# Performance work log

Measured on AMD Instinct MI355X. Metric: run time of the kernel, lower is better.

The kernel has to match this reference:

```python
import jax, jax.numpy as jnp
import numpy as np

NUM_HEADS = 16
HEAD_DIM = 64
HIDDEN = 1024


def setup_inputs() -> dict:
    key = jax.random.key(0)
    ks = jax.random.split(key, 5)
    B, L, D = 1, 2048, HIDDEN
    x = jax.random.normal(ks[0], (B, L, D), dtype=jnp.float32)
    # nn.Linear(D, D, bias=False) weights, stored [out, in] like torch
    sc = 1.0 / np.sqrt(D)
    Wq = jax.random.uniform(ks[1], (D, D), jnp.float32, -sc, sc)
    Wk = jax.random.uniform(ks[2], (D, D), jnp.float32, -sc, sc)
    Wv = jax.random.uniform(ks[3], (D, D), jnp.float32, -sc, sc)
    Wo = jax.random.uniform(ks[4], (D, D), jnp.float32, -sc, sc)
    return {"x": x, "Wq": Wq, "Wk": Wk, "Wv": Wv, "Wo": Wo}


def _entmax_naive(scores_raw, mask):
    # scores_raw: [B,H,L,L] unmasked scaled scores (float32); mask: [L,L] bool (True = future/blocked)
    s = jnp.where(mask, -jnp.inf, scores_raw)
    sorted_s = -jnp.sort(-s, axis=-1)                       # descending
    cumsum = jnp.cumsum(sorted_s, axis=-1)
    k = jnp.arange(1, s.shape[-1] + 1, dtype=jnp.float32)
    tau = (cumsum - 1.0) / k
    k_support = jnp.maximum(
        jnp.sum(sorted_s > tau, axis=-1, keepdims=True), 1
    ).astype(jnp.float32)
    # sum over unmasked entries (the -inf masked entries are excluded)
    s_sum = jnp.sum(jnp.where(mask, 0.0, scores_raw), axis=-1, keepdims=True)
    tau_star = (s_sum - 1.0) / k_support
    p = jnp.where(mask, 0.0, jnp.maximum(scores_raw - tau_star, 0.0))
    return p / (jnp.sum(p, axis=-1, keepdims=True) + 1e-10)


def reference(x, Wq, Wk, Wv, Wo):
    B, L, D = x.shape
    H, hd = NUM_HEADS, HEAD_DIM
    q = jnp.einsum('bld,ed->ble', x, Wq).reshape(B, L, H, hd)
    k = jnp.einsum('bld,ed->ble', x, Wk).reshape(B, L, H, hd)
    v = jnp.einsum('bld,ed->ble', x, Wv).reshape(B, L, H, hd)
    scale = hd ** (-0.5)
    scores = jnp.einsum('bihd,bjhd->bhij', q, k).astype(jnp.float32) * scale
    causal_mask = jnp.triu(jnp.ones((L, L), dtype=bool), 1)
    attn = _entmax_naive(scores, causal_mask)               # [B,H,L,L]
    out = jnp.einsum('bhij,bjhd->bihd', attn.astype(x.dtype), v).reshape(B, L, D)
    return jnp.einsum('bld,ed->ble', out, Wo)
```

## Files before the change

### kernel.cpp

```cpp
#include <hip/hip_runtime.h>
#include <hip/hip_bf16.h>

#define CL 2048
#define CD 1024
#define CH 16
#define CHD 64
#define NEGS -1e30f

typedef __attribute__((ext_vector_type(8))) short short8;
typedef __attribute__((ext_vector_type(4))) float f32x4;
typedef __attribute__((ext_vector_type(32))) float f32x32;

template <int CTRL>
__device__ __forceinline__ float dpp_add_step(float x) {
  int v = __builtin_amdgcn_update_dpp(0, __builtin_bit_cast(int, x),
                                      CTRL, 0xf, 0xf, true);
  return x + __builtin_bit_cast(float, v);
}
template <int CTRL>
__device__ __forceinline__ float dpp_max_step(float x) {
  int v = __builtin_amdgcn_update_dpp((int)0xff800000, __builtin_bit_cast(int, x),
                                      CTRL, 0xf, 0xf, false);
  return fmaxf(x, __builtin_bit_cast(float, v));
}
__device__ __forceinline__ float wave_sum(float x) {
  x = dpp_add_step<0x111>(x);
  x = dpp_add_step<0x112>(x);
  x = dpp_add_step<0x114>(x);
  x = dpp_add_step<0x118>(x);
  x = dpp_add_step<0x142>(x);
  x = dpp_add_step<0x143>(x);
  return __builtin_bit_cast(float,
      __builtin_amdgcn_readlane(__builtin_bit_cast(int, x), 63));
}
__device__ __forceinline__ float wave_max(float x) {
  x = dpp_max_step<0x111>(x);
  x = dpp_max_step<0x112>(x);
  x = dpp_max_step<0x114>(x);
  x = dpp_max_step<0x118>(x);
  x = dpp_max_step<0x142>(x);
  x = dpp_max_step<0x143>(x);
  return __builtin_bit_cast(float,
      __builtin_amdgcn_readlane(__builtin_bit_cast(int, x), 63));
}

__device__ __forceinline__ void split1(float v, short& h, short& l) {
  __hip_bfloat16 bh = __float2bfloat16(v);
  __hip_bfloat16 bl = __float2bfloat16(v - __bfloat162float(bh));
  h = __builtin_bit_cast(short, bh);
  l = __builtin_bit_cast(short, bl);
}
__device__ __forceinline__ unsigned short bf16_bits(float v) {
  __hip_bfloat16 b = __float2bfloat16(v);
  return (unsigned short)__builtin_bit_cast(short, b);
}

__device__ __forceinline__ float tree_sum_valid(const f32x32& s) {
  float t[8];
#pragma unroll
  for (int i = 0; i < 8; i++) {
    const float a = s[i]      > -1e29f ? s[i]      : 0.f;
    const float b = s[i + 8]  > -1e29f ? s[i + 8]  : 0.f;
    const float c = s[i + 16] > -1e29f ? s[i + 16] : 0.f;
    const float d = s[i + 24] > -1e29f ? s[i + 24] : 0.f;
    t[i] = (a + b) + (c + d);
  }
#pragma unroll
  for (int i = 0; i < 4; i++) t[i] += t[i + 4];
  t[0] += t[2]; t[1] += t[3];
  return t[0] + t[1];
}
__device__ __forceinline__ float tree_max(const f32x32& s) {
  float t[8];
#pragma unroll
  for (int i = 0; i < 8; i++)
    t[i] = fmaxf(fmaxf(s[i], s[i + 8]), fmaxf(s[i + 16], s[i + 24]));
#pragma unroll
  for (int i = 0; i < 4; i++) t[i] = fmaxf(t[i], t[i + 4]);
  return fmaxf(fmaxf(t[0], t[2]), fmaxf(t[1], t[3]));
}
__device__ __forceinline__ float relu_store_sum(f32x32& s, float ts_) {
  float t[8];
#pragma unroll
  for (int i = 0; i < 8; i++) {
    float a = s[i] - ts_;      a = a > 0.f ? a : 0.f;
    float b = s[i + 8] - ts_;  b = b > 0.f ? b : 0.f;
    float c = s[i + 16] - ts_; c = c > 0.f ? c : 0.f;
    float d = s[i + 24] - ts_; d = d > 0.f ? d : 0.f;
    s[i] = a; s[i + 8] = b; s[i + 16] = c; s[i + 24] = d;
    t[i] = (a + b) + (c + d);
  }
#pragma unroll
  for (int i = 0; i < 4; i++) t[i] += t[i + 4];
  t[0] += t[2]; t[1] += t[3];
  return t[0] + t[1];
}

__device__ __forceinline__ void entmax_pair(f32x32& s0, f32x32& s1,
                                            int g0, int g1,
                                            float& inv0, float& inv1) {
  const float ss0 = wave_sum(tree_sum_valid(s0));
  const float m0  = wave_max(tree_max(s0));
  const float ss1 = wave_sum(tree_sum_valid(s1));
  const float m1  = wave_max(tree_max(s1));
  float tau0 = m0 - 1.000001f, tau1 = m1 - 1.000001f;
  int cnt0 = 0, cnt1 = 0;
  for (int it = 0; it < 64; it++) {
    float sum0 = 0.f, sum1 = 0.f;
    int c0 = 0, c1 = 0;
#pragma unroll
    for (int jt = 0; jt < 8; jt++) {
      if (jt * 256 <= g0) {
#pragma unroll
        for (int tt = 0; tt < 4; tt++) {
          const float a = s0[jt * 4 + tt];
          const bool pr = a > tau0;
          sum0 += pr ? a : 0.f;
          c0 += (int)__popcll(__ballot(pr));
        }
      }
      if (jt * 256 <= g1) {
#pragma unroll
        for (int tt = 0; tt < 4; tt++) {
          const float a = s1[jt * 4 + tt];
          const bool pr = a > tau1;
          sum1 += pr ? a : 0.f;
          c1 += (int)__popcll(__ballot(pr));
        }
      }
    }
    const float cs0 = wave_sum(sum0);
    const float cs1 = wave_sum(sum1);
    const bool st0 = (c0 == cnt0), st1 = (c1 == cnt1);
    if (st0 && st1) break;
    if (!st0) { cnt0 = c0; tau0 = (cs0 - 1.f) / (float)c0; }
    if (!st1) { cnt1 = c1; tau1 = (cs1 - 1.f) / (float)c1; }
  }
  const float ts0 = (ss0 - 1.f) / (float)cnt0;
  const float ts1 = (ss1 - 1.f) / (float)cnt1;
  inv0 = 1.f / (wave_sum(relu_store_sum(s0, ts0)) + 1e-10f);
  inv1 = 1.f / (wave_sum(relu_store_sum(s1, ts1)) + 1e-10f);
}

__global__ __launch_bounds__(256) void split_all(
    const float* __restrict__ x,  const float* __restrict__ wq,
    const float* __restrict__ wk, const float* __restrict__ wv,
    const float* __restrict__ wo,
    short* __restrict__ xh,  short* __restrict__ xl,
    short* __restrict__ wqh, short* __restrict__ wql,
    short* __restrict__ wkh, short* __restrict__ wkl,
    short* __restrict__ wvh, short* __restrict__ wvl,
    short* __restrict__ woh, short* __restrict__ wol) {
  const int b = blockIdx.x;
  const float* src; short *dh, *dl; int i0;
  if      (b < 2048) { src = x;  dh = xh;  dl = xl;  i0 = b; }
  else if (b < 3072) { src = wq; dh = wqh; dl = wql; i0 = b - 2048; }
  else if (b < 4096) { src = wk; dh = wkh; dl = wkl; i0 = b - 3072; }
  else if (b < 5120) { src = wv; dh = wvh; dl = wvl; i0 = b - 4096; }
  else               { src = wo; dh = woh; dl = wol; i0 = b - 5120; }
  const int i = i0 * 256 + threadIdx.x;
  const float4 v = reinterpret_cast<const float4*>(src)[i];
  const float vv[4] = {v.x, v.y, v.z, v.w};
  short hh[4], ll[4];
#pragma unroll
  for (int e = 0; e < 4; e++) split1(vv[e], hh[e], ll[e]);
  reinterpret_cast<short4*>(dh)[i] = make_short4(hh[0], hh[1], hh[2], hh[3]);
  reinterpret_cast<short4*>(dl)[i] = make_short4(ll[0], ll[1], ll[2], ll[3]);
}

__global__ __launch_bounds__(256, 2) void gemm128_split(
    const short* __restrict__ Ah, const short* __restrict__ Al,
    const short* __restrict__ B0h, const short* __restrict__ B0l,
    const short* __restrict__ B1h, const short* __restrict__ B1l,
    const short* __restrict__ B2h, const short* __restrict__ B2l,
    short* __restrict__ O0h, short* __restrict__ O0l,
    short* __restrict__ O1h, short* __restrict__ O1l,
    short* __restrict__ O2h, short* __restrict__ O2l,
    float* __restrict__ Cf, int fp32out) {
  __shared__ short AhS[128][64], AlS[128][64], BhS[128][64], BlS[128][64];
  const int tid = threadIdx.x, lane = tid & 63, wave = tid >> 6;
  const int l15 = lane & 15, quad = lane >> 4;
  const int sel = blockIdx.x >> 3, nb = blockIdx.x & 7;
  const short* Bh = sel == 0 ? B0h : (sel == 1 ? B1h : B2h);
  const short* Bl = sel == 0 ? B0l : (sel == 1 ? B1l : B2l);
  const int m0 = blockIdx.y * 128, n0 = nb * 128;
  const int wm = (wave >> 1) * 64, wn = (wave & 1) * 64;

  f32x4 acc[4][4];
#pragma unroll
  for (int i = 0; i < 4; i++)
#pragma unroll
    for (int j = 0; j < 4; j++) acc[i][j] = {0.f, 0.f, 0.f, 0.f};

  const short* gsrc = wave == 0 ? Ah : wave == 1 ? Al : wave == 2 ? Bh : Bl;
  short(*ldst)[64] = wave == 0 ? AhS : wave == 1 ? AlS : wave == 2 ? BhS : BlS;
  const int srow0 = (wave < 2) ? m0 : n0;
  const int sr = lane >> 3, skc = (lane & 7) * 8;

  for (int k0 = 0; k0 < CD; k0 += 64) {
#pragma unroll
    for (int i = 0; i < 16; i++) {
      const short* gp =
          gsrc + (size_t)(srow0 + i * 8 + sr) * CD + k0 + skc;
      __builtin_amdgcn_global_load_lds(
          (const __attribute__((address_space(1))) void*)gp,
          (__attribute__((address_space(3))) void*)((char*)&ldst[0][0] + i * 1024),
          16, 0, 0);
    }
    __syncthreads();
#pragma unroll
    for (int kb = 0; kb < 2; kb++) {
      short8 a_h[4], a_l[4], b_h[4], b_l[4];
#pragma unroll
      for (int i = 0; i < 4; i++) {
        a_h[i] = *reinterpret_cast<const short8*>(&AhS[wm + i * 16 + l15][kb * 32 + quad * 8]);
        a_l[i] = *reinterpret_cast<const short8*>(&AlS[wm + i * 16 + l15][kb * 32 + quad * 8]);
        b_h[i] = *reinterpret_cast<const short8*>(&BhS[wn + i * 16 + l15][kb * 32 + quad * 8]);
        b_l[i] = *reinterpret_cast<const short8*>(&BlS[wn + i * 16 + l15][kb * 32 + quad * 8]);
      }
#pragma unroll
      for (int im = 0; im < 4; im++)
#pragma unroll
        for (int in = 0; in < 4; in++) {
          acc[im][in] = __builtin_amdgcn_mfma_f32_16x16x32_bf16(a_h[im], b_l[in], acc[im][in], 0, 0, 0);
          acc[im][in] = __builtin_amdgcn_mfma_f32_16x16x32_bf16(a_l[im], b_h[in], acc[im][in], 0, 0, 0);
          acc[im][in] = __builtin_amdgcn_mfma_f32_16x16x32_bf16(a_h[im], b_h[in], acc[im][in], 0, 0, 0);
        }
    }
    __syncthreads();
  }

#pragma unroll
  for (int im = 0; im < 4; im++)
#pragma unroll
    for (int in = 0; in < 4; in++)
#pragma unroll
      for (int r = 0; r < 4; r++) {
        const int mr = m0 + wm + im * 16 + quad * 4 + r;
        const int nc = n0 + wn + in * 16 + l15;
        const float val = acc[im][in][r];
        if (fp32out) {
          Cf[(size_t)mr * CD + nc] = val;
        } else {
          short sh, sl;
          split1(val, sh, sl);
          if (sel == 0) {
            O0h[(size_t)mr * CD + nc] = sh; O0l[(size_t)mr * CD + nc] = sl;
          } else if (sel == 1) {
            O1h[(size_t)mr * CD + nc] = sh; O1l[(size_t)mr * CD + nc] = sl;
          } else {
            O2h[(size_t)nc * CL + mr] = sh; O2l[(size_t)nc * CL + mr] = sl;
          }
        }
      }
}

__global__ __launch_bounds__(1024, 4) void attn32(
    const short* __restrict__ qh, const short* __restrict__ ql,
    const short* __restrict__ kh, const short* __restrict__ kl,
    const short* __restrict__ vhT, const short* __restrict__ vlT,
    short* __restrict__ oh, short* __restrict__ ol, int qb0) {
  __shared__ float Stile[2][32][260];
  __shared__ unsigned short Ptile[2][32][264];
  __shared__ float Rtile[4][32][68];
  __shared__ float invS[32];

  const int tid = threadIdx.x, lane = tid & 63, wave = tid >> 6;
  const int l15 = lane & 15, quad = lane >> 4;
  const int bx = blockIdx.x;
  const int qb = qb0 + ((bx & 1) ? (31 - (bx >> 1)) : (bx >> 1));
  const int h = blockIdx.y, q0 = qb * 32, col0 = h * CHD;
  const int g0 = q0 + wave;
  const int g1 = q0 + 16 + wave;
  const int ntiles = (q0 + 287) >> 8;
  const int rmax = q0 + 31;

  short8 a0h[2], a0l[2], a1h[2], a1l[2];
  {
    const size_t qbA = (size_t)(q0 + l15) * CD + col0 + quad * 8;
    const size_t qbB = (size_t)(q0 + 16 + l15) * CD + col0 + quad * 8;
#pragma unroll
    for (int kb = 0; kb < 2; kb++) {
      a0h[kb] = *reinterpret_cast<const short8*>(qh + qbA + kb * 32);
      a0l[kb] = *reinterpret_cast<const short8*>(ql + qbA + kb * 32);
      a1h[kb] = *reinterpret_cast<const short8*>(qh + qbB + kb * 32);
      a1l[kb] = *reinterpret_cast<const short8*>(ql + qbB + kb * 32);
    }
  }

  f32x32 s0, s1;
#pragma unroll
  for (int t = 0; t < 32; t++) { s0[t] = NEGS; s1[t] = NEGS; }

#pragma unroll
  for (int jt = 0; jt < 8; jt++) {
    if (jt < ntiles) {
      const int j0 = jt * 256;
      const int buf = jt & 1;
      if (j0 + 16 * wave <= rmax) {
        const size_t kbase = (size_t)(j0 + 16 * wave + l15) * CD + col0 + quad * 8;
        f32x4 c0 = {0.f, 0.f, 0.f, 0.f};
        f32x4 c1 = {0.f, 0.f, 0.f, 0.f};
#pragma unroll
        for (int kb = 0; kb < 2; kb++) {
          const short8 b_h = *reinterpret_cast<const short8*>(kh + kbase + kb * 32);
          const short8 b_l = *reinterpret_cast<const short8*>(kl + kbase + kb * 32);
          c0 = __builtin_amdgcn_mfma_f32_16x16x32_bf16(a0l[kb], b_l, c0, 0, 0, 0);
          c0 = __builtin_amdgcn_mfma_f32_16x16x32_bf16(a0h[kb], b_l, c0, 0, 0, 0);
          c0 = __builtin_amdgcn_mfma_f32_16x16x32_bf16(a0l[kb], b_h, c0, 0, 0, 0);
          c0 = __builtin_amdgcn_mfma_f32_16x16x32_bf16(a0h[kb], b_h, c0, 0, 0, 0);
          c1 = __builtin_amdgcn_mfma_f32_16x16x32_bf16(a1l[kb], b_l, c1, 0, 0, 0);
          c1 = __builtin_amdgcn_mfma_f32_16x16x32_bf16(a1h[kb], b_l, c1, 0, 0, 0);
          c1 = __builtin_amdgcn_mfma_f32_16x16x32_bf16(a1l[kb], b_h, c1, 0, 0, 0);
          c1 = __builtin_amdgcn_mfma_f32_16x16x32_bf16(a1h[kb], b_h, c1, 0, 0, 0);
        }
#pragma unroll
        for (int r = 0; r < 4; r++) {
          Stile[buf][quad * 4 + r][16 * wave + l15] = c0[r];
          Stile[buf][16 + quad * 4 + r][16 * wave + l15] = c1[r];
        }
      }
      __syncthreads();
#pragma unroll
      for (int tt = 0; tt < 4; tt++) {
        const int col = j0 + 64 * tt + lane;
        if (j0 + 64 * tt <= g0) {
          const float v = Stile[buf][wave][64 * tt + lane] * 0.125f;
          s0[jt * 4 + tt] = (col <= g0) ? v : NEGS;
        }
        if (j0 + 64 * tt <= g1) {
          const float v = Stile[buf][wave + 16][64 * tt + lane] * 0.125f;
          s1[jt * 4 + tt] = (col <= g1) ? v : NEGS;
        }
      }
    }
  }

  float inv0, inv1;
  entmax_pair(s0, s1, g0, g1, inv0, inv1);
  if (lane == 0) { invS[wave] = inv0; invS[wave + 16] = inv1; }

  f32x4 acc0 = {0.f, 0.f, 0.f, 0.f};
  f32x4 acc1 = {0.f, 0.f, 0.f, 0.f};
  const int db = wave & 3, kcg = wave >> 2;
#pragma unroll
  for (int jt = 0; jt < 8; jt++) {
    if (jt < ntiles) {
      const int j0 = jt * 256;
      const int buf = jt & 1;
#pragma unroll
      for (int tt = 0; tt < 4; tt++)
        if (j0 + 64 * tt <= rmax) {
          Ptile[buf][wave][64 * tt + lane] = bf16_bits(s0[jt * 4 + tt]);
          Ptile[buf][wave + 16][64 * tt + lane] = bf16_bits(s1[jt * 4 + tt]);
        }
      __syncthreads();
      const size_t vrowbase =
          (size_t)(col0 + 16 * db + l15) * CL + j0;
#pragma unroll
      for (int t2 = 0; t2 < 2; t2++) {
        const int kc = 2 * kcg + t2;
        if (j0 + kc * 32 <= rmax) {
          const short8 pa0 =
              *reinterpret_cast<const short8*>(&Ptile[buf][l15][kc * 32 + quad * 8]);
          const short8 pa1 =
              *reinterpret_cast<const short8*>(&Ptile[buf][l15 + 16][kc * 32 + quad * 8]);
          const size_t vb = vrowbase + kc * 32 + quad * 8;
          const short8 vbh = *reinterpret_cast<const short8*>(vhT + vb);
          const short8 vbl = *reinterpret_cast<const short8*>(vlT + vb);
          acc0 = __builtin_amdgcn_mfma_f32_16x16x32_bf16(pa0, vbl, acc0, 0, 0, 0);
          acc0 = __builtin_amdgcn_mfma_f32_16x16x32_bf16(pa0, vbh, acc0, 0, 0, 0);
          acc1 = __builtin_amdgcn_mfma_f32_16x16x32_bf16(pa1, vbl, acc1, 0, 0, 0);
          acc1 = __builtin_amdgcn_mfma_f32_16x16x32_bf16(pa1, vbh, acc1, 0, 0, 0);
        }
      }
    }
  }

#pragma unroll
  for (int r = 0; r < 4; r++) {
    Rtile[kcg][quad * 4 + r][db * 16 + l15] = acc0[r];
    Rtile[kcg][16 + quad * 4 + r][db * 16 + l15] = acc1[r];
  }
  __syncthreads();
  if (wave < 4) {
#pragma unroll
    for (int r = 0; r < 8; r++) {
      const int row = quad * 8 + r;
      float o = (Rtile[0][row][wave * 16 + l15] + Rtile[1][row][wave * 16 + l15]) +
                (Rtile[2][row][wave * 16 + l15] + Rtile[3][row][wave * 16 + l15]);
      o *= invS[row];
      short sh, sl;
      split1(o, sh, sl);
      const size_t oidx = (size_t)(q0 + row) * CD + col0 + wave * 16 + l15;
      oh[oidx] = sh;
      ol[oidx] = sl;
    }
  }
}

extern "C" void kernel_launch(void* const* d_in, const int* in_sizes, int n_in,
                              void* d_out, int out_size, void* d_ws, size_t ws_size,
                              hipStream_t stream) {
  const float* x  = (const float*)d_in[0];
  const float* Wq = (const float*)d_in[1];
  const float* Wk = (const float*)d_in[2];
  const float* Wv = (const float*)d_in[3];
  const float* Wo = (const float*)d_in[4];
  float* out = (float*)d_out;

  char* ws = (char*)d_ws;
  short* xh  = (short*)(ws + (0ull  << 20));
  short* xl  = (short*)(ws + (4ull  << 20));
  short* wqh = (short*)(ws + (8ull  << 20));
  short* wql = (short*)(ws + (10ull << 20));
  short* wkh = (short*)(ws + (12ull << 20));
  short* wkl = (short*)(ws + (14ull << 20));
  short* wvh = (short*)(ws + (16ull << 20));
  short* wvl = (short*)(ws + (18ull << 20));
  short* woh = (short*)(ws + (20ull << 20));
  short* wol = (short*)(ws + (22ull << 20));
  short* qhp = (short*)(ws + (24ull << 20));
  short* qlp = (short*)(ws + (28ull << 20));
  short* khp = (short*)(ws + (32ull << 20));
  short* klp = (short*)(ws + (36ull << 20));
  short* vhT = (short*)(ws + (40ull << 20));
  short* vlT = (short*)(ws + (44ull << 20));
  short* ohp = (short*)(ws + (48ull << 20));
  short* olp = (short*)(ws + (52ull << 20));

  split_all<<<6144, 256, 0, stream>>>(x, Wq, Wk, Wv, Wo,
                                      xh, xl, wqh, wql, wkh, wkl,
                                      wvh, wvl, woh, wol);

  gemm128_split<<<dim3(24, CL / 128), 256, 0, stream>>>(
      xh, xl, wqh, wql, wkh, wkl, wvh, wvl,
      qhp, qlp, khp, klp, vhT, vlT, nullptr, 0);

  attn32<<<dim3(32, CH), 1024, 0, stream>>>(
      qhp, qlp, khp, klp, vhT, vlT, ohp, olp, 0);
  attn32<<<dim3(32, CH), 1024, 0, stream>>>(
      qhp, qlp, khp, klp, vhT, vlT, ohp, olp, 32);

  gemm128_split<<<dim3(8, CL / 128), 256, 0, stream>>>(
      ohp, olp, woh, wol, woh, wol, woh, wol,
      ohp, olp, ohp, olp, ohp, olp, out, 1);
}
```

Baseline: 386.8 us.

## Prefetch K and V fragments in attention and merge two launches into one

Register-prefetches the next K tile's fragments while the current tile's QK^T MFMAs run. V fragment loads are hoisted ahead of the barrier so they overlap with the P-tile writes and the sync. The two half-grid attention launches become a single 64x16 launch, with a remapped block index that pairs heavy and light causal query blocks for load balance. This costs more live registers, which may hurt occupancy under launch_bounds(1024,4), and removes the split that let the first half's tail overlap with the second launch.

```diff
diff --git a/kernel.cpp b/kernel.cpp
--- a/kernel.cpp
+++ b/kernel.cpp
@@ -259,7 +259,7 @@
     const short* __restrict__ qh, const short* __restrict__ ql,
     const short* __restrict__ kh, const short* __restrict__ kl,
     const short* __restrict__ vhT, const short* __restrict__ vlT,
-    short* __restrict__ oh, short* __restrict__ ol, int qb0) {
+    short* __restrict__ oh, short* __restrict__ ol) {
   __shared__ float Stile[2][32][260];
   __shared__ unsigned short Ptile[2][32][264];
   __shared__ float Rtile[4][32][68];
@@ -268,7 +268,7 @@
   const int tid = threadIdx.x, lane = tid & 63, wave = tid >> 6;
   const int l15 = lane & 15, quad = lane >> 4;
   const int bx = blockIdx.x;
-  const int qb = qb0 + ((bx & 1) ? (31 - (bx >> 1)) : (bx >> 1));
+  const int qb = (bx & 1) ? (63 - (bx >> 1)) : (bx >> 1);
   const int h = blockIdx.y, q0 = qb * 32, col0 = h * CHD;
   const int g0 = q0 + wave;
   const int g1 = q0 + 16 + wave;
@@ -292,27 +292,47 @@
 #pragma unroll
   for (int t = 0; t < 32; t++) { s0[t] = NEGS; s1[t] = NEGS; }
 
+  short8 kfh[2], kfl[2];
+  {
+    if (16 * wave <= rmax) {
+      const size_t kbase = (size_t)(16 * wave + l15) * CD + col0 + quad * 8;
+#pragma unroll
+      for (int kb = 0; kb < 2; kb++) {
+        kfh[kb] = *reinterpret_cast<const short8*>(kh + kbase + kb * 32);
+        kfl[kb] = *reinterpret_cast<const short8*>(kl + kbase + kb * 32);
+      }
+    }
+  }
 #pragma unroll
   for (int jt = 0; jt < 8; jt++) {
     if (jt < ntiles) {
       const int j0 = jt * 256;
       const int buf = jt & 1;
-      if (j0 + 16 * wave <= rmax) {
-        const size_t kbase = (size_t)(j0 + 16 * wave + l15) * CD + col0 + quad * 8;
+      const bool live = (j0 + 16 * wave <= rmax);
+      short8 ch[2], cl[2];
+      if (live) { ch[0] = kfh[0]; ch[1] = kfh[1]; cl[0] = kfl[0]; cl[1] = kfl[1]; }
+      if (jt + 1 < ntiles && (jt + 1) * 256 + 16 * wave <= rmax) {
+        const size_t kb2 =
+            (size_t)((jt + 1) * 256 + 16 * wave + l15) * CD + col0 + quad * 8;
+#pragma unroll
+        for (int kb = 0; kb < 2; kb++) {
+          kfh[kb] = *reinterpret_cast<const short8*>(kh + kb2 + kb * 32);
+          kfl[kb] = *reinterpret_cast<const short8*>(kl + kb2 + kb * 32);
+        }
+      }
+      if (live) {
         f32x4 c0 = {0.f, 0.f, 0.f, 0.f};
         f32x4 c1 = {0.f, 0.f, 0.f, 0.f};
 #pragma unroll
         for (int kb = 0; kb < 2; kb++) {
-          const short8 b_h = *reinterpret_cast<const short8*>(kh + kbase + kb * 32);
-          const short8 b_l = *reinterpret_cast<const short8*>(kl + kbase + kb * 32);
-          c0 = __builtin_amdgcn_mfma_f32_16x16x32_bf16(a0l[kb], b_l, c0, 0, 0, 0);
-          c0 = __builtin_amdgcn_mfma_f32_16x16x32_bf16(a0h[kb], b_l, c0, 0, 0, 0);
-          c0 = __builtin_amdgcn_mfma_f32_16x16x32_bf16(a0l[kb], b_h, c0, 0, 0, 0);
-          c0 = __builtin_amdgcn_mfma_f32_16x16x32_bf16(a0h[kb], b_h, c0, 0, 0, 0);
-          c1 = __builtin_amdgcn_mfma_f32_16x16x32_bf16(a1l[kb], b_l, c1, 0, 0, 0);
-          c1 = __builtin_amdgcn_mfma_f32_16x16x32_bf16(a1h[kb], b_l, c1, 0, 0, 0);
-          c1 = __builtin_amdgcn_mfma_f32_16x16x32_bf16(a1l[kb], b_h, c1, 0, 0, 0);
-          c1 = __builtin_amdgcn_mfma_f32_16x16x32_bf16(a1h[kb], b_h, c1, 0, 0, 0);
+          c0 = __builtin_amdgcn_mfma_f32_16x16x32_bf16(a0l[kb], cl[kb], c0, 0, 0, 0);
+          c0 = __builtin_amdgcn_mfma_f32_16x16x32_bf16(a0h[kb], cl[kb], c0, 0, 0, 0);
+          c0 = __builtin_amdgcn_mfma_f32_16x16x32_bf16(a0l[kb], ch[kb], c0, 0, 0, 0);
+          c0 = __builtin_amdgcn_mfma_f32_16x16x32_bf16(a0h[kb], ch[kb], c0, 0, 0, 0);
+          c1 = __builtin_amdgcn_mfma_f32_16x16x32_bf16(a1l[kb], cl[kb], c1, 0, 0, 0);
+          c1 = __builtin_amdgcn_mfma_f32_16x16x32_bf16(a1h[kb], cl[kb], c1, 0, 0, 0);
+          c1 = __builtin_amdgcn_mfma_f32_16x16x32_bf16(a1l[kb], ch[kb], c1, 0, 0, 0);
+          c1 = __builtin_amdgcn_mfma_f32_16x16x32_bf16(a1h[kb], ch[kb], c1, 0, 0, 0);
         }
 #pragma unroll
         for (int r = 0; r < 4; r++) {
@@ -354,24 +374,32 @@
           Ptile[buf][wave][64 * tt + lane] = bf16_bits(s0[jt * 4 + tt]);
           Ptile[buf][wave + 16][64 * tt + lane] = bf16_bits(s1[jt * 4 + tt]);
         }
-      __syncthreads();
-      const size_t vrowbase =
-          (size_t)(col0 + 16 * db + l15) * CL + j0;
+      const size_t vrowbase = (size_t)(col0 + 16 * db + l15) * CL + j0;
+      short8 vh_[2], vl_[2];
+      bool vlive[2];
 #pragma unroll
       for (int t2 = 0; t2 < 2; t2++) {
         const int kc = 2 * kcg + t2;
-        if (j0 + kc * 32 <= rmax) {
+        vlive[t2] = (j0 + kc * 32 <= rmax);
+        if (vlive[t2]) {
+          const size_t vb = vrowbase + kc * 32 + quad * 8;
+          vh_[t2] = *reinterpret_cast<const short8*>(vhT + vb);
+          vl_[t2] = *reinterpret_cast<const short8*>(vlT + vb);
+        }
+      }
+      __syncthreads();
+#pragma unroll
+      for (int t2 = 0; t2 < 2; t2++) {
+        const int kc = 2 * kcg + t2;
+        if (vlive[t2]) {
           const short8 pa0 =
               *reinterpret_cast<const short8*>(&Ptile[buf][l15][kc * 32 + quad * 8]);
           const short8 pa1 =
               *reinterpret_cast<const short8*>(&Ptile[buf][l15 + 16][kc * 32 + quad * 8]);
-          const size_t vb = vrowbase + kc * 32 + quad * 8;
-          const short8 vbh = *reinterpret_cast<const short8*>(vhT + vb);
-          const short8 vbl = *reinterpret_cast<const short8*>(vlT + vb);
-          acc0 = __builtin_amdgcn_mfma_f32_16x16x32_bf16(pa0, vbl, acc0, 0, 0, 0);
-          acc0 = __builtin_amdgcn_mfma_f32_16x16x32_bf16(pa0, vbh, acc0, 0, 0, 0);
-          acc1 = __builtin_amdgcn_mfma_f32_16x16x32_bf16(pa1, vbl, acc1, 0, 0, 0);
-          acc1 = __builtin_amdgcn_mfma_f32_16x16x32_bf16(pa1, vbh, acc1, 0, 0, 0);
+          acc0 = __builtin_amdgcn_mfma_f32_16x16x32_bf16(pa0, vl_[t2], acc0, 0, 0, 0);
+          acc0 = __builtin_amdgcn_mfma_f32_16x16x32_bf16(pa0, vh_[t2], acc0, 0, 0, 0);
+          acc1 = __builtin_amdgcn_mfma_f32_16x16x32_bf16(pa1, vl_[t2], acc1, 0, 0, 0);
+          acc1 = __builtin_amdgcn_mfma_f32_16x16x32_bf16(pa1, vh_[t2], acc1, 0, 0, 0);
         }
       }
     }
@@ -437,10 +465,8 @@
       xh, xl, wqh, wql, wkh, wkl, wvh, wvl,
       qhp, qlp, khp, klp, vhT, vlT, nullptr, 0);
 
-  attn32<<<dim3(32, CH), 1024, 0, stream>>>(
-      qhp, qlp, khp, klp, vhT, vlT, ohp, olp, 0);
-  attn32<<<dim3(32, CH), 1024, 0, stream>>>(
-      qhp, qlp, khp, klp, vhT, vlT, ohp, olp, 32);
+  attn32<<<dim3(CL / 32, CH), 1024, 0, stream>>>(
+      qhp, qlp, khp, klp, vhT, vlT, ohp, olp);
 
   gemm128_split<<<dim3(8, CL / 128), 256, 0, stream>>>(
       ohp, olp, woh, wol, woh, wol, woh, wol,
```

Result: slower. 477.6 us (+23.5%).
